# Kernel tuning notes

Hardware: AMD Instinct MI355X
Metric: run time of the kernel (lower is better)

## Reference

```python
import jax, jax.numpy as jnp
import numpy as np

B, S, D = 2, 2048, 512
H = 8
HD = D // H  # head dim = 64


def setup_inputs() -> dict:
    key = jax.random.key(0)
    ks = jax.random.split(key, 4)
    scale = 1.0 / np.sqrt(D)
    x = jax.random.normal(ks[0], (B, S, D), dtype=jnp.float32)
    wq = jax.random.normal(ks[1], (D, D), dtype=jnp.float32) * scale
    wk = jax.random.normal(ks[2], (D, D), dtype=jnp.float32) * scale
    wv = jax.random.normal(ks[3], (D, D), dtype=jnp.float32) * scale
    bq = jnp.zeros((D,), dtype=jnp.float32)
    bk = jnp.zeros((D,), dtype=jnp.float32)
    bv = jnp.zeros((D,), dtype=jnp.float32)
    return {"x": x, "wq": wq, "bq": bq, "wk": wk, "bk": bk, "wv": wv, "bv": bv}


def reference(x, wq, bq, wk, bk, wv, bv):
    # Linear projections (torch Linear: y = x @ W^T + b; weights here stored as [out,in])
    q = x @ wq.T + bq  # [B,S,D]
    k = x @ wk.T + bk
    v = x @ wv.T + bv
    # split heads -> [B,H,S,HD]
    q = q.reshape(B, S, H, HD).transpose(0, 2, 1, 3)
    k = k.reshape(B, S, H, HD).transpose(0, 2, 1, 3)
    v = v.reshape(B, S, H, HD).transpose(0, 2, 1, 3)
    # QK^T scores, scaled by 1/sqrt(head_dim)
    scores = jnp.einsum("bhqd,bhkd->bhqk", q, k) / jnp.sqrt(jnp.float32(HD))
    # softmax-free: elementwise sigmoid instead of softmax normalization
    attn = jax.nn.sigmoid(scores)  # [B,H,S,S] — the memory-bound intermediate
    out = jnp.einsum("bhqk,bhkd->bhqd", attn, v)
    # merge heads -> [B,S,D]
    return out.transpose(0, 2, 1, 3).reshape(B, S, D)
```

## Files before the change

kernel.cpp:

```cpp
#include <hip/hip_runtime.h>
#include <cstdint>
#include <cstddef>

#define BB   2
#define SS   2048
#define DD   512
#define HH   8
#define HDIM 64

typedef __attribute__((ext_vector_type(8)))  short          s16x8;
typedef __attribute__((ext_vector_type(16))) float          f32x16;

static __device__ __forceinline__ unsigned short f2bf(float f) {
  union { float f; unsigned u; } x; x.f = f;
  unsigned r = x.u + 0x7fffu + ((x.u >> 16) & 1u);
  return (unsigned short)(r >> 16);
}
static __device__ __forceinline__ unsigned packtrunc(float lo, float hi) {
  return __builtin_amdgcn_perm(__float_as_uint(hi), __float_as_uint(lo), 0x07060302u);
}

#define QSCALE (-0.18033688011111543f)

__global__ __launch_bounds__(256) void proj_kernel(
    const float* __restrict__ x,
    const float* __restrict__ wq, const float* __restrict__ wk, const float* __restrict__ wv,
    const float* __restrict__ bq, const float* __restrict__ bk, const float* __restrict__ bv,
    unsigned short* __restrict__ qo, unsigned short* __restrict__ ko,
    unsigned short* __restrict__ vt) {
  __shared__ unsigned short As[2][64 * 40];
  __shared__ unsigned short Bs[2][64 * 40];

  const int z = blockIdx.z;
  const float* w; const float* bias;
  if (z == 0)      { w = wq; bias = bq; }
  else if (z == 1) { w = wk; bias = bk; }
  else             { w = wv; bias = bv; }

  const int t = threadIdx.x;
  const int lane = t & 63, wave = t >> 6;
  const int ln = lane & 31, hi = lane >> 5;
  const int wr = wave >> 1, wc = wave & 1;
  const int m0 = blockIdx.x * 64, n0 = blockIdx.y * 64;

  float4 ar[2], br[2];
#pragma unroll
  for (int i = 0; i < 2; i++) {
    int c = t + i * 256;
    ar[i] = *(const float4*)&x[(size_t)(m0 + (c >> 3)) * DD + (c & 7) * 4];
    br[i] = *(const float4*)&w[(size_t)(n0 + (c >> 3)) * DD + (c & 7) * 4];
  }
#pragma unroll
  for (int i = 0; i < 2; i++) {
    int c = t + i * 256;
    uint2 ua, ub;
    ua.x = packtrunc(ar[i].x, ar[i].y); ua.y = packtrunc(ar[i].z, ar[i].w);
    ub.x = packtrunc(br[i].x, br[i].y); ub.y = packtrunc(br[i].z, br[i].w);
    *(uint2*)&As[0][(c >> 3) * 40 + (c & 7) * 4] = ua;
    *(uint2*)&Bs[0][(c >> 3) * 40 + (c & 7) * 4] = ub;
  }
  __syncthreads();

  f32x16 acc = {};

#pragma unroll 2
  for (int kt = 0; kt < 16; kt++) {
    const int cur = kt & 1, nxt = cur ^ 1;
    if (kt < 15) {
      int k0 = (kt + 1) * 32;
#pragma unroll
      for (int i = 0; i < 2; i++) {
        int c = t + i * 256;
        ar[i] = *(const float4*)&x[(size_t)(m0 + (c >> 3)) * DD + k0 + (c & 7) * 4];
        br[i] = *(const float4*)&w[(size_t)(n0 + (c >> 3)) * DD + k0 + (c & 7) * 4];
      }
    }
#pragma unroll
    for (int c = 0; c < 2; c++) {
      s16x8 af = *(const s16x8*)&As[cur][(wr * 32 + ln) * 40 + c * 16 + hi * 8];
      s16x8 bf = *(const s16x8*)&Bs[cur][(wc * 32 + ln) * 40 + c * 16 + hi * 8];
      acc = __builtin_amdgcn_mfma_f32_32x32x16_bf16(af, bf, acc, 0, 0, 0);
    }
    if (kt < 15) {
#pragma unroll
      for (int i = 0; i < 2; i++) {
        int c = t + i * 256;
        uint2 ua, ub;
        ua.x = packtrunc(ar[i].x, ar[i].y); ua.y = packtrunc(ar[i].z, ar[i].w);
        ub.x = packtrunc(br[i].x, br[i].y); ub.y = packtrunc(br[i].z, br[i].w);
        *(uint2*)&As[nxt][(c >> 3) * 40 + (c & 7) * 4] = ua;
        *(uint2*)&Bs[nxt][(c >> 3) * 40 + (c & 7) * 4] = ub;
      }
    }
    __syncthreads();
  }

  const int h = blockIdx.y;
  const int bidx = m0 >> 11;
  const int sbase = (m0 & 2047) + wr * 32;
  const int hd = wc * 32 + ln;
  const float bval = bias[n0 + hd];
  const size_t bhb = (size_t)(bidx * HH + h) * SS * HDIM;

  if (z == 0) {
#pragma unroll
    for (int r = 0; r < 16; r++) {
      int s = sbase + (r & 3) + 8 * (r >> 2) + 4 * hi;
      qo[bhb + (size_t)s * HDIM + hd] = f2bf((acc[r] + bval) * QSCALE);
    }
  } else if (z == 1) {
    const int c = hd >> 4, hk = (hd >> 3) & 1, j = hd & 7;
    const int kts = sbase >> 5;
    unsigned short* kd = ko + bhb + ((size_t)kts * 4 + c) * 512 + j;
#pragma unroll
    for (int r = 0; r < 16; r++) {
      int off = (r & 3) + 8 * (r >> 2) + 4 * hi;
      kd[(hk * 32 + off) * 8] = f2bf(acc[r] + bval);
    }
  } else {
    const int kts = sbase >> 5;
    unsigned short* vd = vt + bhb + ((size_t)kts * 4 + wc * 2) * 512 + hi * 256 + ln * 8;
#pragma unroll
    for (int g = 0; g < 4; g++) {
      unsigned short* vg = vd + (g >> 1) * 512 + (g & 1) * 4;
#pragma unroll
      for (int j = 0; j < 4; j += 2) {
        unsigned pk = (unsigned)f2bf(acc[g * 4 + j] + bval) |
                      ((unsigned)f2bf(acc[g * 4 + j + 1] + bval) << 16);
        *(unsigned*)&vg[j] = pk;
      }
    }
  }
}

__global__ __launch_bounds__(256, 2) void attn_kernel(
    const unsigned short* __restrict__ qb,
    const unsigned short* __restrict__ kfb,
    const unsigned short* __restrict__ vfb,
    float* __restrict__ out) {
  __shared__ __align__(16) float red[2][2048];

  const int t = threadIdx.x;
  const int lane = t & 63, wave = t >> 6;
  const int ln = lane & 31, hi = lane >> 5;
  const int fid = blockIdx.y * 64 + blockIdx.x;
  const int bh = fid & 15, qx = fid >> 4;
  const int b = bh >> 3, h = bh & 7;
  const unsigned short* qp = qb + (size_t)bh * SS * HDIM;
  const unsigned short* kfp = kfb + (size_t)bh * SS * HDIM;
  const unsigned short* vfp = vfb + (size_t)bh * SS * HDIM;
  const int q0 = qx * 32;

  s16x8 qf[4];
#pragma unroll
  for (int c = 0; c < 4; c++)
    qf[c] = *(const s16x8*)&qp[(size_t)(q0 + ln) * HDIM + c * 16 + hi * 8];

  f32x16 o0 = {}, o1 = {};

  s16x8 kf[2][4], vf[2][4];
  int foff = wave * 4 * 512 + lane * 8;
#pragma unroll
  for (int c = 0; c < 4; c++) {
    kf[0][c] = *(const s16x8*)&kfp[foff + c * 512];
    vf[0][c] = *(const s16x8*)&vfp[foff + c * 512];
  }
  foff += 8192;

#pragma unroll 2
  for (int i = 0; i < 16; i++) {
    const int cur = i & 1, nxt = cur ^ 1;
    if (i < 15) {
#pragma unroll
      for (int c = 0; c < 4; c++) {
        kf[nxt][c] = *(const s16x8*)&kfp[foff + c * 512];
        vf[nxt][c] = *(const s16x8*)&vfp[foff + c * 512];
      }
      foff += 8192;
    }

    f32x16 st = {};
#pragma unroll
    for (int c = 0; c < 4; c++)
      st = __builtin_amdgcn_mfma_f32_32x32x16_bf16(kf[cur][c], qf[c], st, 0, 0, 0);

    unsigned pg[8];
#pragma unroll
    for (int g = 0; g < 4; g++) {
      float p0 = __builtin_amdgcn_rcpf(1.0f + __builtin_amdgcn_exp2f(st[4 * g + 0]));
      float p1 = __builtin_amdgcn_rcpf(1.0f + __builtin_amdgcn_exp2f(st[4 * g + 1]));
      float p2 = __builtin_amdgcn_rcpf(1.0f + __builtin_amdgcn_exp2f(st[4 * g + 2]));
      float p3 = __builtin_amdgcn_rcpf(1.0f + __builtin_amdgcn_exp2f(st[4 * g + 3]));
      pg[2 * g]     = packtrunc(p0, p1);
      pg[2 * g + 1] = packtrunc(p2, p3);
    }

#pragma unroll
    for (int c = 0; c < 2; c++) {
      union { unsigned u[4]; s16x8 v; } pu;
      pu.u[0] = pg[4 * c + 0];
      pu.u[1] = pg[4 * c + 1];
      pu.u[2] = pg[4 * c + 2];
      pu.u[3] = pg[4 * c + 3];
      o0 = __builtin_amdgcn_mfma_f32_32x32x16_bf16(pu.v, vf[cur][c], o0, 0, 0, 0);
      o1 = __builtin_amdgcn_mfma_f32_32x32x16_bf16(pu.v, vf[cur][2 + c], o1, 0, 0, 0);
    }
  }

  if (wave >= 2) {
#pragma unroll
    for (int dh = 0; dh < 2; dh++) {
      f32x16 ov = dh ? o1 : o0;
#pragma unroll
      for (int r = 0; r < 16; r++) {
        int ql = (r & 3) + 8 * (r >> 2) + 4 * hi;
        red[wave - 2][ql * 64 + dh * 32 + ln] = ov[r];
      }
    }
  }
  __syncthreads();
  if (wave < 2) {
#pragma unroll
    for (int dh = 0; dh < 2; dh++) {
      f32x16 ov = dh ? o1 : o0;
#pragma unroll
      for (int r = 0; r < 16; r++) {
        int ql = (r & 3) + 8 * (r >> 2) + 4 * hi;
        red[wave][ql * 64 + dh * 32 + ln] += ov[r];
      }
    }
  }
  __syncthreads();
  const float4* r0 = (const float4*)&red[0][0];
  const float4* r1 = (const float4*)&red[1][0];
#pragma unroll
  for (int j = 0; j < 2; j++) {
    int g = t + j * 256;
    float4 s0 = r0[g], s1 = r1[g];
    float4 s;
    s.x = s0.x + s1.x; s.y = s0.y + s1.y; s.z = s0.z + s1.z; s.w = s0.w + s1.w;
    int q = g >> 4, dbase = (g & 15) * 4;
    *(float4*)&out[((size_t)(b * SS + q0 + q)) * DD + h * HDIM + dbase] = s;
  }
}

extern "C" void kernel_launch(void* const* d_in, const int* in_sizes, int n_in,
                              void* d_out, int out_size, void* d_ws, size_t ws_size,
                              hipStream_t stream) {
  const float* x  = (const float*)d_in[0];
  const float* wq = (const float*)d_in[1];
  const float* bq = (const float*)d_in[2];
  const float* wk = (const float*)d_in[3];
  const float* bk = (const float*)d_in[4];
  const float* wv = (const float*)d_in[5];
  const float* bv = (const float*)d_in[6];
  float* out = (float*)d_out;

  constexpr size_t XN = (size_t)BB * SS * DD;

  unsigned short* qo = (unsigned short*)d_ws;
  unsigned short* ko = qo + XN;
  unsigned short* vt = ko + XN;

  proj_kernel<<<dim3(64, 8, 3), 256, 0, stream>>>(x, wq, wk, wv, bq, bk, bv, qo, ko, vt);
  attn_kernel<<<dim3(SS / 32, BB * HH), 256, 0, stream>>>(qo, ko, vt, out);
}
```

Before: 117.3 us.

## Widen attention block to 64 queries with 8 waves and contiguous key ranges

The attention kernel now uses 512 threads per block covering 64 queries. Waves are split into two query halves and four key-range quarters, each quarter walking a contiguous stretch of keys instead of an interleaved stride. The double-buffered K/V registers are replaced by single buffers that are reloaded right after each is consumed, and the loop is no longer unrolled, which cuts register pressure but exposes more load latency. The grid halves, so each K/V tile is shared by two query groups, while the shared-memory reduction buffer doubles in size.

```diff
diff --git a/kernel.cpp b/kernel.cpp
--- a/kernel.cpp
+++ b/kernel.cpp
@@ -133,56 +133,53 @@
   }
 }
 
-__global__ __launch_bounds__(256, 2) void attn_kernel(
+__global__ __launch_bounds__(512, 2) void attn_kernel(
     const unsigned short* __restrict__ qb,
     const unsigned short* __restrict__ kfb,
     const unsigned short* __restrict__ vfb,
     float* __restrict__ out) {
-  __shared__ __align__(16) float red[2][2048];
+  __shared__ __align__(16) float red[2 * 4096];
 
   const int t = threadIdx.x;
   const int lane = t & 63, wave = t >> 6;
   const int ln = lane & 31, hi = lane >> 5;
-  const int fid = blockIdx.y * 64 + blockIdx.x;
+  const int qh = wave & 1, kh = wave >> 1;
+  const int fid = blockIdx.y * 32 + blockIdx.x;
   const int bh = fid & 15, qx = fid >> 4;
   const int b = bh >> 3, h = bh & 7;
   const unsigned short* qp = qb + (size_t)bh * SS * HDIM;
   const unsigned short* kfp = kfb + (size_t)bh * SS * HDIM;
   const unsigned short* vfp = vfb + (size_t)bh * SS * HDIM;
-  const int q0 = qx * 32;
+  const int q0 = qx * 64;
 
   s16x8 qf[4];
 #pragma unroll
   for (int c = 0; c < 4; c++)
-    qf[c] = *(const s16x8*)&qp[(size_t)(q0 + ln) * HDIM + c * 16 + hi * 8];
+    qf[c] = *(const s16x8*)&qp[(size_t)(q0 + qh * 32 + ln) * HDIM + c * 16 + hi * 8];
 
   f32x16 o0 = {}, o1 = {};
 
-  s16x8 kf[2][4], vf[2][4];
-  int foff = wave * 4 * 512 + lane * 8;
+  s16x8 kf[4], vf[4];
+  int foff = kh * 16 * 2048 + lane * 8;
 #pragma unroll
   for (int c = 0; c < 4; c++) {
-    kf[0][c] = *(const s16x8*)&kfp[foff + c * 512];
-    vf[0][c] = *(const s16x8*)&vfp[foff + c * 512];
-  }
-  foff += 8192;
-
-#pragma unroll 2
+    kf[c] = *(const s16x8*)&kfp[foff + c * 512];
+    vf[c] = *(const s16x8*)&vfp[foff + c * 512];
+  }
+  foff += 2048;
+
+#pragma unroll 1
   for (int i = 0; i < 16; i++) {
-    const int cur = i & 1, nxt = cur ^ 1;
+    f32x16 st = {};
+#pragma unroll
+    for (int c = 0; c < 4; c++)
+      st = __builtin_amdgcn_mfma_f32_32x32x16_bf16(kf[c], qf[c], st, 0, 0, 0);
+
     if (i < 15) {
 #pragma unroll
-      for (int c = 0; c < 4; c++) {
-        kf[nxt][c] = *(const s16x8*)&kfp[foff + c * 512];
-        vf[nxt][c] = *(const s16x8*)&vfp[foff + c * 512];
-      }
-      foff += 8192;
-    }
-
-    f32x16 st = {};
-#pragma unroll
-    for (int c = 0; c < 4; c++)
-      st = __builtin_amdgcn_mfma_f32_32x32x16_bf16(kf[cur][c], qf[c], st, 0, 0, 0);
+      for (int c = 0; c < 4; c++)
+        kf[c] = *(const s16x8*)&kfp[foff + c * 512];
+    }
 
     unsigned pg[8];
 #pragma unroll
@@ -202,40 +199,48 @@
       pu.u[1] = pg[4 * c + 1];
       pu.u[2] = pg[4 * c + 2];
       pu.u[3] = pg[4 * c + 3];
-      o0 = __builtin_amdgcn_mfma_f32_32x32x16_bf16(pu.v, vf[cur][c], o0, 0, 0, 0);
-      o1 = __builtin_amdgcn_mfma_f32_32x32x16_bf16(pu.v, vf[cur][2 + c], o1, 0, 0, 0);
-    }
-  }
-
-  if (wave >= 2) {
+      o0 = __builtin_amdgcn_mfma_f32_32x32x16_bf16(pu.v, vf[c], o0, 0, 0, 0);
+      o1 = __builtin_amdgcn_mfma_f32_32x32x16_bf16(pu.v, vf[2 + c], o1, 0, 0, 0);
+    }
+
+    if (i < 15) {
+#pragma unroll
+      for (int c = 0; c < 4; c++)
+        vf[c] = *(const s16x8*)&vfp[foff + c * 512];
+      foff += 2048;
+    }
+  }
+
+  if (kh >= 2) {
+    const int slot = kh - 2;
 #pragma unroll
     for (int dh = 0; dh < 2; dh++) {
       f32x16 ov = dh ? o1 : o0;
 #pragma unroll
       for (int r = 0; r < 16; r++) {
         int ql = (r & 3) + 8 * (r >> 2) + 4 * hi;
-        red[wave - 2][ql * 64 + dh * 32 + ln] = ov[r];
+        red[slot * 4096 + (qh * 32 + ql) * 64 + dh * 32 + ln] = ov[r];
       }
     }
   }
   __syncthreads();
-  if (wave < 2) {
+  if (kh < 2) {
 #pragma unroll
     for (int dh = 0; dh < 2; dh++) {
       f32x16 ov = dh ? o1 : o0;
 #pragma unroll
       for (int r = 0; r < 16; r++) {
         int ql = (r & 3) + 8 * (r >> 2) + 4 * hi;
-        red[wave][ql * 64 + dh * 32 + ln] += ov[r];
+        red[kh * 4096 + (qh * 32 + ql) * 64 + dh * 32 + ln] += ov[r];
       }
     }
   }
   __syncthreads();
-  const float4* r0 = (const float4*)&red[0][0];
-  const float4* r1 = (const float4*)&red[1][0];
+  const float4* r0 = (const float4*)red;
+  const float4* r1 = (const float4*)(red + 4096);
 #pragma unroll
   for (int j = 0; j < 2; j++) {
-    int g = t + j * 256;
+    int g = t + j * 512;
     float4 s0 = r0[g], s1 = r1[g];
     float4 s;
     s.x = s0.x + s1.x; s.y = s0.y + s1.y; s.z = s0.z + s1.z; s.w = s0.w + s1.w;
@@ -263,5 +268,5 @@
   unsigned short* vt = ko + XN;
 
   proj_kernel<<<dim3(64, 8, 3), 256, 0, stream>>>(x, wq, wk, wv, bq, bk, bv, qo, ko, vt);
-  attn_kernel<<<dim3(SS / 32, BB * HH), 256, 0, stream>>>(qo, ko, vt, out);
-}
+  attn_kernel<<<dim3(SS / 64, BB * HH), 512, 0, stream>>>(qo, ko, vt, out);
+}
```

After: 116.1 us. About the same (-1.0%).
